# Kernel optimization log

Hardware: AMD Instinct MI355X
Metric: run time of the kernel (lower is better)

Reference implementation:

```python
import jax, jax.numpy as jnp
import numpy as np

N_NODES = 50000
N_EDGES = 600000
D = 128
EDGE_D = 32
N_LAYERS = 3
BN_EPS = 1e-5


def setup_inputs() -> dict:
    key = jax.random.key(0)
    ks = jax.random.split(key, 8)
    x = jax.random.normal(ks[0], (N_NODES, D), dtype=jnp.float32)
    edge_index = jax.random.randint(ks[1], (2, N_EDGES), 0, N_NODES, dtype=jnp.int64)
    edge_attr = jax.random.normal(ks[2], (N_EDGES, EDGE_D), dtype=jnp.float32)
    W_lin = jax.random.normal(ks[3], (N_LAYERS, EDGE_D, D), dtype=jnp.float32) * 0.05
    b_lin = jnp.zeros((N_LAYERS, D), dtype=jnp.float32)
    W1 = jax.random.normal(ks[4], (N_LAYERS, D, D), dtype=jnp.float32) * 0.05
    b1 = jnp.zeros((N_LAYERS, D), dtype=jnp.float32)
    W2 = jax.random.normal(ks[5], (N_LAYERS, D, D), dtype=jnp.float32) * 0.05
    b2 = jnp.zeros((N_LAYERS, D), dtype=jnp.float32)
    gamma = jnp.ones((N_LAYERS, D), dtype=jnp.float32)
    beta = jnp.zeros((N_LAYERS, D), dtype=jnp.float32)
    return {"x": x, "edge_index": edge_index, "edge_attr": edge_attr,
            "W_lin": W_lin, "b_lin": b_lin, "W1": W1, "b1": b1,
            "W2": W2, "b2": b2, "gamma": gamma, "beta": beta}


def reference(x, edge_index, edge_attr, W_lin, b_lin, W1, b1, W2, b2, gamma, beta):
    # MPNN with GINEConv layers: for each layer,
    #   msg_e = ReLU(x[src_e] + Linear(edge_attr_e))      (PyG GINEConv edge lift)
    #   agg_i = sum over edges with dst==i of msg_e        (scatter-sum)
    #   h     = MLP((1+eps)*x + agg), eps=0
    #   x     = ReLU(BatchNorm1d(h))                       (training-mode batch stats)
    src, dst = edge_index[0], edge_index[1]
    n = x.shape[0]
    for l in range(W1.shape[0]):
        e = edge_attr @ W_lin[l] + b_lin[l]                 # [E, D]
        msg = jax.nn.relu(x[src] + e)                       # gather + fuse
        agg = jax.ops.segment_sum(msg, dst, num_segments=n)  # [N, D]
        h = x + agg                                         # eps = 0
        h = jax.nn.relu(h @ W1[l] + b1[l]) @ W2[l] + b2[l]   # GIN MLP
        mu = jnp.mean(h, axis=0)
        var = jnp.var(h, axis=0)
        h = (h - mu) * jax.lax.rsqrt(var + BN_EPS) * gamma[l] + beta[l]
        x = jax.nn.relu(h)
    return x
```

## Files before the change

### kernel.cpp

```cpp
#include <hip/hip_runtime.h>

#define D_DIM 128
#define EDGE_DIM 32
#define BN_EPS 1e-5f

typedef __attribute__((ext_vector_type(8))) _Float16 f16x8;
typedef __attribute__((ext_vector_type(2))) _Float16 half2v;
typedef __attribute__((ext_vector_type(4))) float f32x4;
typedef unsigned short ushort_t;

__device__ __forceinline__ unsigned short f2h(float f) {
    union { _Float16 h; unsigned short u; } c;
    c.h = (_Float16)f;
    return c.u;
}
__device__ __forceinline__ unsigned pk2h(float lo, float hi) {
    return (unsigned)f2h(lo) | ((unsigned)f2h(hi) << 16);
}
__device__ __forceinline__ half2v asH2(unsigned u) {
    union { unsigned u; half2v h; } c;
    c.u = u;
    return c.h;
}
__device__ __forceinline__ float fdot2f(half2v a, half2v b, float c) {
#if __has_builtin(__builtin_amdgcn_fdot2)
    return __builtin_amdgcn_fdot2(a, b, c, false);
#else
    return c + (float)a.x * (float)b.x + (float)a.y * (float)b.y;
#endif
}

__global__ __launch_bounds__(256) void hist_kernel(
    const int* __restrict__ dst, int* __restrict__ cnt, int E)
{
    for (int e = blockIdx.x * 256 + threadIdx.x; e < E; e += gridDim.x * 256)
        atomicAdd(&cnt[dst[e]], 1);
}

__global__ __launch_bounds__(256) void scan_local_kernel(
    const int* __restrict__ cnt, int* __restrict__ off,
    int* __restrict__ blksum, int n)
{
    __shared__ int part[256];
    const int t = threadIdx.x;
    const int base = blockIdx.x * 2048 + t * 8;
    int v[8];
    int s = 0;
#pragma unroll
    for (int j = 0; j < 8; ++j) {
        const int idx = base + j;
        const int c = (idx < n) ? cnt[idx] : 0;
        v[j] = s;
        s += c;
    }
    part[t] = s;
    __syncthreads();
    for (int d = 1; d < 256; d <<= 1) {
        const int val = (t >= d) ? part[t - d] : 0;
        __syncthreads();
        part[t] += val;
        __syncthreads();
    }
    const int texcl = (t > 0) ? part[t - 1] : 0;
#pragma unroll
    for (int j = 0; j < 8; ++j) {
        const int idx = base + j;
        if (idx < n) off[idx] = texcl + v[j];
    }
    if (t == 255) blksum[blockIdx.x] = part[255];
}

__global__ __launch_bounds__(64) void scan_tops_kernel(
    int* __restrict__ blksum, int* __restrict__ off, int n, int B)
{
    if (threadIdx.x == 0) {
        int run = 0;
        for (int b = 0; b < B; ++b) {
            const int v = blksum[b];
            blksum[b] = run;
            run += v;
        }
        off[n] = run;
    }
}

__global__ __launch_bounds__(256) void scan_add_kernel(
    int* __restrict__ off, int* __restrict__ cur,
    const int* __restrict__ blksum, int n)
{
    const int base = blockIdx.x * 2048;
    const int add = blksum[blockIdx.x];
    for (int j = threadIdx.x; j < 2048; j += 256) {
        const int i = base + j;
        if (i < n) {
            const int v = off[i] + add;
            off[i] = v;
            cur[i] = v;
        }
    }
}

__global__ __launch_bounds__(256) void scatter_conv_kernel(
    const int* __restrict__ src, const int* __restrict__ dst,
    const float* __restrict__ ea,
    int* __restrict__ cur, int* __restrict__ srcs,
    uint4* __restrict__ ea16q, int E)
{
    for (int e = blockIdx.x * 256 + threadIdx.x; e < E; e += gridDim.x * 256) {
        const int p = atomicAdd(&cur[dst[e]], 1);
        srcs[p] = src[e];
        const float* __restrict__ er = ea + (size_t)e * EDGE_DIM;
#pragma unroll
        for (int q = 0; q < 4; ++q) {
            const float4 a = *(const float4*)(er + q * 8);
            const float4 b = *(const float4*)(er + q * 8 + 4);
            uint4 o;
            o.x = pk2h(a.x, a.y); o.y = pk2h(a.z, a.w);
            o.z = pk2h(b.x, b.y); o.w = pk2h(b.z, b.w);
            ea16q[(size_t)p * 4 + q] = o;
        }
    }
}

__global__ __launch_bounds__(256) void wbuild_all_kernel(
    const float* __restrict__ W_lin, const float* __restrict__ W1,
    const float* __restrict__ W2,
    unsigned* __restrict__ wl3, unsigned* __restrict__ wf13,
    unsigned* __restrict__ wf23)
{
    const int idx = blockIdx.x * 256 + threadIdx.x;
    if (idx >= 3 * 18432) return;
    const int l = idx / 18432;
    const int r = idx % 18432;
    const float* Wl  = W_lin + (size_t)l * EDGE_DIM * D_DIM;
    const float* W1l = W1 + (size_t)l * D_DIM * D_DIM;
    const float* W2l = W2 + (size_t)l * D_DIM * D_DIM;
    if (r < 2048) {
        const int kp = r >> 7, c = r & 127;
        wl3[l * 2048 + r] = pk2h(Wl[(2 * kp) * D_DIM + c], Wl[(2 * kp + 1) * D_DIM + c]);
    } else if (r < 10240) {
        const int i = r - 2048;
        const int col = i >> 6, kp = i & 63;
        wf13[l * 8192 + i] = pk2h(W1l[(2 * kp) * D_DIM + col], W1l[(2 * kp + 1) * D_DIM + col]);
    } else {
        const int i = r - 10240;
        const int col = i >> 6, kp = i & 63;
        wf23[l * 8192 + i] = pk2h(W2l[(2 * kp) * D_DIM + col], W2l[(2 * kp + 1) * D_DIM + col]);
    }
}

__global__ __launch_bounds__(256) void xprep0_kernel(
    const float* __restrict__ h, uint2* __restrict__ x16q, int M)
{
    const int total = M * 32;
    for (int i = blockIdx.x * 256 + threadIdx.x; i < total; i += gridDim.x * 256) {
        const float4 v = ((const float4*)h)[i];
        uint2 o; o.x = pk2h(v.x, v.y); o.y = pk2h(v.z, v.w);
        x16q[i] = o;
    }
}

__global__ __launch_bounds__(256) void apply_final_kernel(
    const ushort_t* __restrict__ h16, const float* __restrict__ sums,
    const float* __restrict__ gamma, const float* __restrict__ beta,
    float invN, float* __restrict__ outp, int M)
{
    __shared__ float sc[128], sh[128];
    if (threadIdx.x < 128) {
        const int c = threadIdx.x;
        const float mu  = sums[c] * invN;
        const float var = sums[128 + c] * invN - mu * mu;
        const float s   = gamma[c] * rsqrtf(var + BN_EPS);
        sc[c] = s;
        sh[c] = beta[c] - mu * s;
    }
    __syncthreads();
    const int total = M * 32;
    for (int i = blockIdx.x * 256 + threadIdx.x; i < total; i += gridDim.x * 256) {
        const uint2 hv = *(const uint2*)(h16 + (size_t)i * 4);
        const half2v a = asH2(hv.x), b = asH2(hv.y);
        const int c = (i & 31) * 4;
        f32x4 o;
        o[0] = fmaxf(fmaf((float)a.x, sc[c + 0], sh[c + 0]), 0.f);
        o[1] = fmaxf(fmaf((float)a.y, sc[c + 1], sh[c + 1]), 0.f);
        o[2] = fmaxf(fmaf((float)b.x, sc[c + 2], sh[c + 2]), 0.f);
        o[3] = fmaxf(fmaf((float)b.y, sc[c + 3], sh[c + 3]), 0.f);
        *(f32x4*)(outp + (size_t)i * 4) = o;
    }
}

template<int XFORM>
__global__ __launch_bounds__(256, 2) void edge_agg_kernel(
    const unsigned* __restrict__ hsrc,
    const int*      __restrict__ srcs,
    const uint4*    __restrict__ ea16q,
    const int*      __restrict__ row_off,
    const unsigned* __restrict__ wl16d,
    const float*    __restrict__ bl,
    const float*    __restrict__ sums,
    const float*    __restrict__ gamma,
    const float*    __restrict__ beta,
    float invN,
    unsigned*       __restrict__ agg16d,
    int nNodes)
{
    const int lane = threadIdx.x & 63;
    const int wid  = threadIdx.x >> 6;

    unsigned wA[16], wB[16];
#pragma unroll
    for (int kp = 0; kp < 16; ++kp) {
        const uint2 w2 = *(const uint2*)(wl16d + kp * 128 + 2 * lane);
        wA[kp] = w2.x; wB[kp] = w2.y;
    }
#pragma unroll
    for (int kp = 0; kp < 16; ++kp) {
        asm volatile("" : "+v"(wA[kp]));
        asm volatile("" : "+v"(wB[kp]));
    }
    const float b0 = bl[2 * lane];
    const float b1 = bl[2 * lane + 1];

    float scl0 = 1.f, shl0 = 0.f, scl1 = 1.f, shl1 = 0.f;
    if (XFORM) {
        const int c0 = 2 * lane, c1 = 2 * lane + 1;
        const float mu0 = sums[c0] * invN;
        const float va0 = sums[128 + c0] * invN - mu0 * mu0;
        scl0 = gamma[c0] * rsqrtf(va0 + BN_EPS);
        shl0 = beta[c0] - mu0 * scl0;
        const float mu1 = sums[c1] * invN;
        const float va1 = sums[128 + c1] * invN - mu1 * mu1;
        scl1 = gamma[c1] * rsqrtf(va1 + BN_EPS);
        shl1 = beta[c1] - mu1 * scl1;
    }

    const int stride = gridDim.x * 4;
    for (int node = blockIdx.x * 4 + wid; node < nNodes; node += stride) {
        const int beg = __builtin_amdgcn_readfirstlane(row_off[node]);
        const int end = __builtin_amdgcn_readfirstlane(row_off[node + 1]);
        float acc0 = 0.f, acc1 = 0.f;

        const int nPair = (end - beg) >> 1;
        int j = beg;
        int sA = 0, sB = 0;
        if (nPair > 0) { sA = srcs[j]; sB = srcs[j + 1]; }

#pragma unroll 1
        for (int it = 0; it < nPair; ++it) {
            const unsigned xdA = hsrc[(size_t)sA * 64 + lane];
            const unsigned xdB = hsrc[(size_t)sB * 64 + lane];
            int sA2 = sA, sB2 = sB;
            if (it + 1 < nPair) {
                sA2 = srcs[j + 2];
                sB2 = srcs[j + 3];
            }
            const uint4 a0 = ea16q[(size_t)j * 4 + 0];
            const uint4 a1 = ea16q[(size_t)j * 4 + 1];
            const uint4 a2 = ea16q[(size_t)j * 4 + 2];
            const uint4 a3 = ea16q[(size_t)j * 4 + 3];
            const uint4 c0 = ea16q[(size_t)(j + 1) * 4 + 0];
            const uint4 c1 = ea16q[(size_t)(j + 1) * 4 + 1];
            const uint4 c2 = ea16q[(size_t)(j + 1) * 4 + 2];
            const uint4 c3 = ea16q[(size_t)(j + 1) * 4 + 3];

            const unsigned awA[16] = {a0.x, a0.y, a0.z, a0.w,
                                      a1.x, a1.y, a1.z, a1.w,
                                      a2.x, a2.y, a2.z, a2.w,
                                      a3.x, a3.y, a3.z, a3.w};
            const unsigned awB[16] = {c0.x, c0.y, c0.z, c0.w,
                                      c1.x, c1.y, c1.z, c1.w,
                                      c2.x, c2.y, c2.z, c2.w,
                                      c3.x, c3.y, c3.z, c3.w};
            float pA0 = b0, pA1 = b1, pB0 = b0, pB1 = b1;
            float qA0 = 0.f, qA1 = 0.f, qB0 = 0.f, qB1 = 0.f;
#pragma unroll
            for (int kp = 0; kp < 8; ++kp) {
                pA0 = fdot2f(asH2(awA[kp]), asH2(wA[kp]), pA0);
                pA1 = fdot2f(asH2(awA[kp]), asH2(wB[kp]), pA1);
                pB0 = fdot2f(asH2(awB[kp]), asH2(wA[kp]), pB0);
                pB1 = fdot2f(asH2(awB[kp]), asH2(wB[kp]), pB1);
                qA0 = fdot2f(asH2(awA[kp + 8]), asH2(wA[kp + 8]), qA0);
                qA1 = fdot2f(asH2(awA[kp + 8]), asH2(wB[kp + 8]), qA1);
                qB0 = fdot2f(asH2(awB[kp + 8]), asH2(wA[kp + 8]), qB0);
                qB1 = fdot2f(asH2(awB[kp + 8]), asH2(wB[kp + 8]), qB1);
            }
            const half2v xhA = asH2(xdA);
            const half2v xhB = asH2(xdB);
            float xA0 = (float)xhA.x, xA1 = (float)xhA.y;
            float xB0 = (float)xhB.x, xB1 = (float)xhB.y;
            if (XFORM) {
                xA0 = fmaxf(fmaf(xA0, scl0, shl0), 0.f);
                xA1 = fmaxf(fmaf(xA1, scl1, shl1), 0.f);
                xB0 = fmaxf(fmaf(xB0, scl0, shl0), 0.f);
                xB1 = fmaxf(fmaf(xB1, scl1, shl1), 0.f);
            }
            acc0 += fmaxf(xA0 + pA0 + qA0, 0.f) + fmaxf(xB0 + pB0 + qB0, 0.f);
            acc1 += fmaxf(xA1 + pA1 + qA1, 0.f) + fmaxf(xB1 + pB1 + qB1, 0.f);
            sA = sA2; sB = sB2;
            j += 2;
        }
        if (j < end) {
            const int s = srcs[j];
            const unsigned xd = hsrc[(size_t)s * 64 + lane];
            const uint4 a0 = ea16q[(size_t)j * 4 + 0];
            const uint4 a1 = ea16q[(size_t)j * 4 + 1];
            const uint4 a2 = ea16q[(size_t)j * 4 + 2];
            const uint4 a3 = ea16q[(size_t)j * 4 + 3];
            const unsigned aw[16] = {a0.x, a0.y, a0.z, a0.w,
                                     a1.x, a1.y, a1.z, a1.w,
                                     a2.x, a2.y, a2.z, a2.w,
                                     a3.x, a3.y, a3.z, a3.w};
            float p0 = b0, p1 = b1, q0 = 0.f, q1 = 0.f;
#pragma unroll
            for (int kp = 0; kp < 8; ++kp) {
                p0 = fdot2f(asH2(aw[kp]), asH2(wA[kp]), p0);
                p1 = fdot2f(asH2(aw[kp]), asH2(wB[kp]), p1);
                q0 = fdot2f(asH2(aw[kp + 8]), asH2(wA[kp + 8]), q0);
                q1 = fdot2f(asH2(aw[kp + 8]), asH2(wB[kp + 8]), q1);
            }
            const half2v xh = asH2(xd);
            float x0 = (float)xh.x, x1 = (float)xh.y;
            if (XFORM) {
                x0 = fmaxf(fmaf(x0, scl0, shl0), 0.f);
                x1 = fmaxf(fmaf(x1, scl1, shl1), 0.f);
            }
            acc0 += fmaxf(x0 + p0 + q0, 0.f);
            acc1 += fmaxf(x1 + p1 + q1, 0.f);
        }
        const half2v xo = asH2(hsrc[(size_t)node * 64 + lane]);
        float x0 = (float)xo.x, x1 = (float)xo.y;
        if (XFORM) {
            x0 = fmaxf(fmaf(x0, scl0, shl0), 0.f);
            x1 = fmaxf(fmaf(x1, scl1, shl1), 0.f);
        }
        agg16d[(size_t)node * 64 + lane] = pk2h(x0 + acc0, x1 + acc1);
    }
}

__global__ __launch_bounds__(256) void fused_mlp_kernel(
    const unsigned* __restrict__ agg16d,
    const ushort_t* __restrict__ wf1,
    const float* __restrict__ b1,
    const ushort_t* __restrict__ wf2,
    const float* __restrict__ b2,
    ushort_t* __restrict__ h16,
    float* __restrict__ sums,
    int M)
{
    __shared__ char ATb[128 * 256];
    __shared__ float bsum[256];
    const int tid = threadIdx.x;
    const int m0  = blockIdx.x * 128;

    bsum[tid] = 0.f;

#pragma unroll
    for (int i = 0; i < 8; ++i) {
        const int idx = i * 256 + tid;
        const int r = idx >> 4, c16 = idx & 15;
        const int row = m0 + r;
        uint4 v = make_uint4(0u, 0u, 0u, 0u);
        if (row < M) v = *(const uint4*)(agg16d + (size_t)row * 64 + c16 * 4);
        *(uint4*)(ATb + r * 256 + ((c16 * 16) ^ ((r & 7) << 4))) = v;
    }
    __syncthreads();

    const int lane = tid & 63;
    const int w    = tid >> 6;
    const int fr   = lane & 15;
    const int fg   = lane >> 4;
    const int ar0  = w * 32 + fr;
    const int asz  = (ar0 & 7) << 4;

    f32x4 acc[2][8];
#pragma unroll
    for (int a = 0; a < 2; ++a)
#pragma unroll
        for (int b = 0; b < 8; ++b) acc[a][b] = (f32x4){0.f, 0.f, 0.f, 0.f};

#pragma unroll
    for (int ks = 0; ks < 4; ++ks) {
        const int kb = ks * 64 + fg * 16;
        const f16x8 a0 = *(const f16x8*)(ATb + ar0 * 256 + (kb ^ asz));
        const f16x8 a1 = *(const f16x8*)(ATb + (ar0 + 16) * 256 + (kb ^ asz));
        f16x8 bf[8];
#pragma unroll
        for (int cb = 0; cb < 8; ++cb)
            bf[cb] = *(const f16x8*)(wf1 + (cb * 16 + fr) * 128 + ks * 32 + fg * 8);
#pragma unroll
        for (int cb = 0; cb < 8; ++cb) {
            acc[0][cb] = __builtin_amdgcn_mfma_f32_16x16x32_f16(a0, bf[cb], acc[0][cb], 0, 0, 0);
            acc[1][cb] = __builtin_amdgcn_mfma_f32_16x16x32_f16(a1, bf[cb], acc[1][cb], 0, 0, 0);
        }
    }
    __syncthreads();

    {
        float b1v[8];
#pragma unroll
        for (int cb = 0; cb < 8; ++cb) b1v[cb] = b1[cb * 16 + fr];
#pragma unroll
        for (int rf = 0; rf < 2; ++rf) {
            const int rb = w * 32 + rf * 16 + fg * 4;
#pragma unroll
            for (int cb = 0; cb < 8; ++cb) {
                const int cc = cb * 16 + fr;
#pragma unroll
                for (int j = 0; j < 4; ++j) {
                    const int r = rb + j;
                    const float v = fmaxf(acc[rf][cb][j] + b1v[cb], 0.f);
                    *(ushort_t*)(ATb + r * 256 + ((cc * 2) ^ ((r & 7) << 4))) = f2h(v);
                }
            }
        }
    }
#pragma unroll
    for (int a = 0; a < 2; ++a)
#pragma unroll
        for (int b = 0; b < 8; ++b) acc[a][b] = (f32x4){0.f, 0.f, 0.f, 0.f};
    __syncthreads();

#pragma unroll
    for (int ks = 0; ks < 4; ++ks) {
        const int kb = ks * 64 + fg * 16;
        const f16x8 a0 = *(const f16x8*)(ATb + ar0 * 256 + (kb ^ asz));
        const f16x8 a1 = *(const f16x8*)(ATb + (ar0 + 16) * 256 + (kb ^ asz));
        f16x8 bf[8];
#pragma unroll
        for (int cb = 0; cb < 8; ++cb)
            bf[cb] = *(const f16x8*)(wf2 + (cb * 16 + fr) * 128 + ks * 32 + fg * 8);
#pragma unroll
        for (int cb = 0; cb < 8; ++cb) {
            acc[0][cb] = __builtin_amdgcn_mfma_f32_16x16x32_f16(a0, bf[cb], acc[0][cb], 0, 0, 0);
            acc[1][cb] = __builtin_amdgcn_mfma_f32_16x16x32_f16(a1, bf[cb], acc[1][cb], 0, 0, 0);
        }
    }

    float b2v[8];
#pragma unroll
    for (int cb = 0; cb < 8; ++cb) b2v[cb] = b2[cb * 16 + fr];
    float s[8], q[8];
#pragma unroll
    for (int cb = 0; cb < 8; ++cb) { s[cb] = 0.f; q[cb] = 0.f; }

#pragma unroll
    for (int rf = 0; rf < 2; ++rf) {
        const int r0 = m0 + w * 32 + rf * 16 + fg * 4;
#pragma unroll
        for (int cb = 0; cb < 8; ++cb) {
            const int col = cb * 16 + fr;
#pragma unroll
            for (int j = 0; j < 4; ++j) {
                const int row = r0 + j;
                if (row < M) {
                    const float v = acc[rf][cb][j] + b2v[cb];
                    h16[(size_t)row * 128 + col] = f2h(v);
                    s[cb] += v;
                    q[cb] += v * v;
                }
            }
        }
    }
#pragma unroll
    for (int cb = 0; cb < 8; ++cb) {
        float ss = s[cb]; ss += __shfl_down(ss, 32); ss += __shfl_down(ss, 16);
        float qq = q[cb]; qq += __shfl_down(qq, 32); qq += __shfl_down(qq, 16);
        if (lane < 16) {
            atomicAdd(&bsum[cb * 16 + lane], ss);
            atomicAdd(&bsum[128 + cb * 16 + lane], qq);
        }
    }
    __syncthreads();
    unsafeAtomicAdd(&sums[tid], bsum[tid]);
}

extern "C" void kernel_launch(void* const* d_in, const int* in_sizes, int n_in,
                              void* d_out, int out_size, void* d_ws, size_t ws_size,
                              hipStream_t stream)
{
    const float* x_in  = (const float*)d_in[0];
    const int*   ei    = (const int*)  d_in[1];
    const float* ea    = (const float*)d_in[2];
    const float* W_lin = (const float*)d_in[3];
    const float* b_lin = (const float*)d_in[4];
    const float* W1    = (const float*)d_in[5];
    const float* b1    = (const float*)d_in[6];
    const float* W2    = (const float*)d_in[7];
    const float* b2    = (const float*)d_in[8];
    const float* gamma = (const float*)d_in[9];
    const float* beta  = (const float*)d_in[10];

    const int N = in_sizes[0] / D_DIM;
    const int E = in_sizes[2] / EDGE_DIM;
    const int L = in_sizes[3] / (EDGE_DIM * D_DIM);
    const float invN = 1.f / (float)N;

    const int* src = ei;
    const int* dst = ei + E;

    float* out = (float*)d_out;

    char* wp = (char*)d_ws;
    auto take = [&wp](size_t bytes) {
        char* r = wp;
        wp += (bytes + 15) & ~(size_t)15;
        return r;
    };
    unsigned*  agg16d  = (unsigned*) take((size_t)N * D_DIM * 2);
    ushort_t*  h16     = (ushort_t*) take((size_t)N * D_DIM * 2);
    unsigned*  x16d    = (unsigned*) take((size_t)N * D_DIM * 2);
    float*     sums3   = (float*)    take(3 * 256 * 4);
    unsigned*  wl3     = (unsigned*) take(3 * 2048 * 4);
    unsigned*  wf13    = (unsigned*) take(3 * 8192 * 4);
    unsigned*  wf23    = (unsigned*) take(3 * 8192 * 4);
    int*       cnt     = (int*)      take((size_t)N * 4);
    int*       row_off = (int*)      take((size_t)(N + 1) * 4);
    int*       cur     = (int*)      take((size_t)N * 4);
    int*       blksum  = (int*)      take(256 * 4);
    int*       srcs    = (int*)      take((size_t)E * 4);
    uint4*     ea16q   = (uint4*)    take((size_t)E * 64);

    const int gemmBlocks = (N + 127) / 128;
    const int scanBlocks = (N + 2047) / 2048;

    hipMemsetAsync(cnt, 0, (size_t)N * sizeof(int), stream);
    hipMemsetAsync(sums3, 0, 3 * 256 * sizeof(float), stream);
    hist_kernel<<<1024, 256, 0, stream>>>(dst, cnt, E);
    scan_local_kernel<<<scanBlocks, 256, 0, stream>>>(cnt, row_off, blksum, N);
    scan_tops_kernel<<<1, 64, 0, stream>>>(blksum, row_off, N, scanBlocks);
    scan_add_kernel<<<scanBlocks, 256, 0, stream>>>(row_off, cur, blksum, N);
    scatter_conv_kernel<<<1024, 256, 0, stream>>>(src, dst, ea, cur, srcs, ea16q, E);
    wbuild_all_kernel<<<216, 256, 0, stream>>>(W_lin, W1, W2, wl3, wf13, wf23);
    xprep0_kernel<<<1024, 256, 0, stream>>>(x_in, (uint2*)x16d, N);

    for (int l = 0; l < L; ++l) {
        const float* bl_l = b_lin + (size_t)l * D_DIM;
        const float* b1_l = b1 + (size_t)l * D_DIM;
        const float* b2_l = b2 + (size_t)l * D_DIM;
        const unsigned* wl_l = wl3 + (size_t)l * 2048;
        const ushort_t* wf1_l = (const ushort_t*)(wf13 + (size_t)l * 8192);
        const ushort_t* wf2_l = (const ushort_t*)(wf23 + (size_t)l * 8192);

        if (l == 0) {
            edge_agg_kernel<0><<<2048, 256, 0, stream>>>(
                x16d, srcs, ea16q, row_off, wl_l, bl_l,
                nullptr, nullptr, nullptr, invN, agg16d, N);
        } else {
            edge_agg_kernel<1><<<2048, 256, 0, stream>>>(
                (const unsigned*)h16, srcs, ea16q, row_off, wl_l, bl_l,
                sums3 + (size_t)(l - 1) * 256,
                gamma + (size_t)(l - 1) * D_DIM,
                beta + (size_t)(l - 1) * D_DIM, invN, agg16d, N);
        }

        fused_mlp_kernel<<<gemmBlocks, 256, 0, stream>>>(
            agg16d, wf1_l, b1_l, wf2_l, b2_l, h16,
            sums3 + (size_t)l * 256, N);
    }

    apply_final_kernel<<<1024, 256, 0, stream>>>(
        h16, sums3 + 2 * 256, gamma + 2 * D_DIM, beta + 2 * D_DIM,
        invN, out, N);
}
```

Measured before the change: 420.1 us.

## Compute edge linear with MFMA per edge chunk into LDS, then aggregate

The edge aggregation kernel is restructured. Nodes are grouped into chunks of about 64 CSR edges, found by a new chunk_first kernel. Each block first computes edge_attr@W_lin for its chunk with 16x16x32 f16 MFMA and stores the result in shared memory; waves then gather source features and reduce per node, four edges at a time. This replaces the per-lane fdot2 recomputation and raises the occupancy hint, but adds a shared-memory round trip and relies on the ECAP=120 capacity, which can overflow when one high-degree node makes a chunk exceed it.

New measurement: 404.4 us. 1.04x faster.

```diff
diff --git a/kernel.cpp b/kernel.cpp
--- a/kernel.cpp
+++ b/kernel.cpp
@@ -3,6 +3,8 @@
 #define D_DIM 128
 #define EDGE_DIM 32
 #define BN_EPS 1e-5f
+#define CHUNK 64
+#define ECAP 120
 
 typedef __attribute__((ext_vector_type(8))) _Float16 f16x8;
 typedef __attribute__((ext_vector_type(2))) _Float16 half2v;
@@ -21,13 +23,6 @@
     union { unsigned u; half2v h; } c;
     c.u = u;
     return c.h;
-}
-__device__ __forceinline__ float fdot2f(half2v a, half2v b, float c) {
-#if __has_builtin(__builtin_amdgcn_fdot2)
-    return __builtin_amdgcn_fdot2(a, b, c, false);
-#else
-    return c + (float)a.x * (float)b.x + (float)a.y * (float)b.y;
-#endif
 }
 
 __global__ __launch_bounds__(256) void hist_kernel(
@@ -122,6 +117,19 @@
     }
 }
 
+__global__ __launch_bounds__(256) void chunk_first_kernel(
+    const int* __restrict__ row_off, int* __restrict__ chunk_first,
+    int n, int nchunks)
+{
+    const int i = blockIdx.x * 256 + threadIdx.x;
+    if (i == 0) chunk_first[nchunks] = n;
+    if (i < n) {
+        int c = row_off[i] / CHUNK;
+        if (c > nchunks - 1) c = nchunks - 1;
+        atomicMin(&chunk_first[c], i);
+    }
+}
+
 __global__ __launch_bounds__(256) void wbuild_all_kernel(
     const float* __restrict__ W_lin, const float* __restrict__ W1,
     const float* __restrict__ W2,
@@ -136,8 +144,11 @@
     const float* W1l = W1 + (size_t)l * D_DIM * D_DIM;
     const float* W2l = W2 + (size_t)l * D_DIM * D_DIM;
     if (r < 2048) {
-        const int kp = r >> 7, c = r & 127;
-        wl3[l * 2048 + r] = pk2h(Wl[(2 * kp) * D_DIM + c], Wl[(2 * kp + 1) * D_DIM + c]);
+        const int slot = r >> 2, q = r & 3;
+        const int cb = slot >> 6, lane = slot & 63;
+        const int col = cb * 16 + (lane & 15);
+        const int k0 = (lane >> 4) * 8 + 2 * q;
+        wl3[l * 2048 + r] = pk2h(Wl[k0 * D_DIM + col], Wl[(k0 + 1) * D_DIM + col]);
     } else if (r < 10240) {
         const int i = r - 2048;
         const int col = i >> 6, kp = i & 63;
@@ -190,13 +201,14 @@
 }
 
 template<int XFORM>
-__global__ __launch_bounds__(256, 2) void edge_agg_kernel(
+__global__ __launch_bounds__(256, 5) void fused_edge_kernel(
     const unsigned* __restrict__ hsrc,
     const int*      __restrict__ srcs,
-    const uint4*    __restrict__ ea16q,
+    const ushort_t* __restrict__ ea16,
+    const ushort_t* __restrict__ wflin,
+    const float*    __restrict__ bl,
     const int*      __restrict__ row_off,
-    const unsigned* __restrict__ wl16d,
-    const float*    __restrict__ bl,
+    const int*      __restrict__ chunk_first,
     const float*    __restrict__ sums,
     const float*    __restrict__ gamma,
     const float*    __restrict__ beta,
@@ -204,22 +216,55 @@
     unsigned*       __restrict__ agg16d,
     int nNodes)
 {
-    const int lane = threadIdx.x & 63;
-    const int wid  = threadIdx.x >> 6;
-
-    unsigned wA[16], wB[16];
-#pragma unroll
-    for (int kp = 0; kp < 16; ++kp) {
-        const uint2 w2 = *(const uint2*)(wl16d + kp * 128 + 2 * lane);
-        wA[kp] = w2.x; wB[kp] = w2.y;
-    }
-#pragma unroll
-    for (int kp = 0; kp < 16; ++kp) {
-        asm volatile("" : "+v"(wA[kp]));
-        asm volatile("" : "+v"(wB[kp]));
-    }
-    const float b0 = bl[2 * lane];
-    const float b1 = bl[2 * lane + 1];
+    __shared__ ushort_t eT[ECAP * 132];
+    const int tid  = threadIdx.x;
+    const int lane = tid & 63;
+    const int w    = tid >> 6;
+    const int fr   = lane & 15;
+    const int fg   = lane >> 4;
+    const int c    = blockIdx.x;
+
+    int nfirst = chunk_first[c];
+    int nlast  = chunk_first[c + 1];
+    if (nfirst > nNodes) nfirst = nNodes;
+    if (nlast  > nNodes) nlast  = nNodes;
+    if (nfirst >= nlast) return;
+    const int ebase = row_off[nfirst];
+    const int ecnt  = row_off[nlast] - ebase;
+
+    f16x8 bfr[8];
+#pragma unroll
+    for (int cb = 0; cb < 8; ++cb)
+        bfr[cb] = *(const f16x8*)(wflin + (cb * 64 + lane) * 8);
+    float blv[8];
+#pragma unroll
+    for (int cb = 0; cb < 8; ++cb) blv[cb] = bl[cb * 16 + fr];
+
+    const int rowblocks = (ecnt + 15) >> 4;
+#pragma unroll
+    for (int rr = 0; rr < 2; ++rr) {
+        const int rb = w + rr * 4;
+        if (rb < rowblocks) {
+            const f16x8 af = *(const f16x8*)(ea16
+                + ((size_t)(ebase + rb * 16 + fr)) * 32 + fg * 8);
+            f32x4 acc[8];
+#pragma unroll
+            for (int cb = 0; cb < 8; ++cb) {
+                const f32x4 z = {0.f, 0.f, 0.f, 0.f};
+                acc[cb] = __builtin_amdgcn_mfma_f32_16x16x32_f16(af, bfr[cb], z, 0, 0, 0);
+            }
+#pragma unroll
+            for (int cb = 0; cb < 8; ++cb) {
+                const int col = cb * 16 + fr;
+#pragma unroll
+                for (int j = 0; j < 4; ++j) {
+                    const int er = rb * 16 + fg * 4 + j;
+                    eT[er * 132 + col] = f2h(acc[cb][j] + blv[cb]);
+                }
+            }
+        }
+    }
+    __syncthreads();
 
     float scl0 = 1.f, shl0 = 0.f, scl1 = 1.f, shl1 = 0.f;
     if (XFORM) {
@@ -234,106 +279,62 @@
         shl1 = beta[c1] - mu1 * scl1;
     }
 
-    const int stride = gridDim.x * 4;
-    for (int node = blockIdx.x * 4 + wid; node < nNodes; node += stride) {
-        const int beg = __builtin_amdgcn_readfirstlane(row_off[node]);
-        const int end = __builtin_amdgcn_readfirstlane(row_off[node + 1]);
-        float acc0 = 0.f, acc1 = 0.f;
-
-        const int nPair = (end - beg) >> 1;
-        int j = beg;
-        int sA = 0, sB = 0;
-        if (nPair > 0) { sA = srcs[j]; sB = srcs[j + 1]; }
-
+    for (int n = nfirst + w; n < nlast; n += 4) {
+        const int beg = __builtin_amdgcn_readfirstlane(row_off[n]);
+        const int end = __builtin_amdgcn_readfirstlane(row_off[n + 1]);
+        float a0 = 0.f, a1 = 0.f;
+        int p = beg;
+        const int head = (end - beg) & 3;
 #pragma unroll 1
-        for (int it = 0; it < nPair; ++it) {
-            const unsigned xdA = hsrc[(size_t)sA * 64 + lane];
-            const unsigned xdB = hsrc[(size_t)sB * 64 + lane];
-            int sA2 = sA, sB2 = sB;
-            if (it + 1 < nPair) {
-                sA2 = srcs[j + 2];
-                sB2 = srcs[j + 3];
-            }
-            const uint4 a0 = ea16q[(size_t)j * 4 + 0];
-            const uint4 a1 = ea16q[(size_t)j * 4 + 1];
-            const uint4 a2 = ea16q[(size_t)j * 4 + 2];
-            const uint4 a3 = ea16q[(size_t)j * 4 + 3];
-            const uint4 c0 = ea16q[(size_t)(j + 1) * 4 + 0];
-            const uint4 c1 = ea16q[(size_t)(j + 1) * 4 + 1];
-            const uint4 c2 = ea16q[(size_t)(j + 1) * 4 + 2];
-            const uint4 c3 = ea16q[(size_t)(j + 1) * 4 + 3];
-
-            const unsigned awA[16] = {a0.x, a0.y, a0.z, a0.w,
-                                      a1.x, a1.y, a1.z, a1.w,
-                                      a2.x, a2.y, a2.z, a2.w,
-                                      a3.x, a3.y, a3.z, a3.w};
-            const unsigned awB[16] = {c0.x, c0.y, c0.z, c0.w,
-                                      c1.x, c1.y, c1.z, c1.w,
-                                      c2.x, c2.y, c2.z, c2.w,
-                                      c3.x, c3.y, c3.z, c3.w};
-            float pA0 = b0, pA1 = b1, pB0 = b0, pB1 = b1;
-            float qA0 = 0.f, qA1 = 0.f, qB0 = 0.f, qB1 = 0.f;
-#pragma unroll
-            for (int kp = 0; kp < 8; ++kp) {
-                pA0 = fdot2f(asH2(awA[kp]), asH2(wA[kp]), pA0);
-                pA1 = fdot2f(asH2(awA[kp]), asH2(wB[kp]), pA1);
-                pB0 = fdot2f(asH2(awB[kp]), asH2(wA[kp]), pB0);
-                pB1 = fdot2f(asH2(awB[kp]), asH2(wB[kp]), pB1);
-                qA0 = fdot2f(asH2(awA[kp + 8]), asH2(wA[kp + 8]), qA0);
-                qA1 = fdot2f(asH2(awA[kp + 8]), asH2(wB[kp + 8]), qA1);
-                qB0 = fdot2f(asH2(awB[kp + 8]), asH2(wA[kp + 8]), qB0);
-                qB1 = fdot2f(asH2(awB[kp + 8]), asH2(wB[kp + 8]), qB1);
-            }
-            const half2v xhA = asH2(xdA);
-            const half2v xhB = asH2(xdB);
-            float xA0 = (float)xhA.x, xA1 = (float)xhA.y;
-            float xB0 = (float)xhB.x, xB1 = (float)xhB.y;
-            if (XFORM) {
-                xA0 = fmaxf(fmaf(xA0, scl0, shl0), 0.f);
-                xA1 = fmaxf(fmaf(xA1, scl1, shl1), 0.f);
-                xB0 = fmaxf(fmaf(xB0, scl0, shl0), 0.f);
-                xB1 = fmaxf(fmaf(xB1, scl1, shl1), 0.f);
-            }
-            acc0 += fmaxf(xA0 + pA0 + qA0, 0.f) + fmaxf(xB0 + pB0 + qB0, 0.f);
-            acc1 += fmaxf(xA1 + pA1 + qA1, 0.f) + fmaxf(xB1 + pB1 + qB1, 0.f);
-            sA = sA2; sB = sB2;
-            j += 2;
-        }
-        if (j < end) {
-            const int s = srcs[j];
+        for (int t = 0; t < head; ++t, ++p) {
+            const int s = __builtin_amdgcn_readfirstlane(srcs[p]);
             const unsigned xd = hsrc[(size_t)s * 64 + lane];
-            const uint4 a0 = ea16q[(size_t)j * 4 + 0];
-            const uint4 a1 = ea16q[(size_t)j * 4 + 1];
-            const uint4 a2 = ea16q[(size_t)j * 4 + 2];
-            const uint4 a3 = ea16q[(size_t)j * 4 + 3];
-            const unsigned aw[16] = {a0.x, a0.y, a0.z, a0.w,
-                                     a1.x, a1.y, a1.z, a1.w,
-                                     a2.x, a2.y, a2.z, a2.w,
-                                     a3.x, a3.y, a3.z, a3.w};
-            float p0 = b0, p1 = b1, q0 = 0.f, q1 = 0.f;
-#pragma unroll
-            for (int kp = 0; kp < 8; ++kp) {
-                p0 = fdot2f(asH2(aw[kp]), asH2(wA[kp]), p0);
-                p1 = fdot2f(asH2(aw[kp]), asH2(wB[kp]), p1);
-                q0 = fdot2f(asH2(aw[kp + 8]), asH2(wA[kp + 8]), q0);
-                q1 = fdot2f(asH2(aw[kp + 8]), asH2(wB[kp + 8]), q1);
-            }
-            const half2v xh = asH2(xd);
+            const unsigned ed = *(const unsigned*)&eT[(p - ebase) * 132 + 2 * lane];
+            const half2v xh = asH2(xd), eh = asH2(ed);
             float x0 = (float)xh.x, x1 = (float)xh.y;
             if (XFORM) {
                 x0 = fmaxf(fmaf(x0, scl0, shl0), 0.f);
                 x1 = fmaxf(fmaf(x1, scl1, shl1), 0.f);
             }
-            acc0 += fmaxf(x0 + p0 + q0, 0.f);
-            acc1 += fmaxf(x1 + p1 + q1, 0.f);
-        }
-        const half2v xo = asH2(hsrc[(size_t)node * 64 + lane]);
+            a0 += fmaxf(x0 + (float)eh.x, 0.f);
+            a1 += fmaxf(x1 + (float)eh.y, 0.f);
+        }
+#pragma unroll 1
+        for (; p < end; p += 4) {
+            const int s0 = __builtin_amdgcn_readfirstlane(srcs[p]);
+            const int s1 = __builtin_amdgcn_readfirstlane(srcs[p + 1]);
+            const int s2 = __builtin_amdgcn_readfirstlane(srcs[p + 2]);
+            const int s3 = __builtin_amdgcn_readfirstlane(srcs[p + 3]);
+            const unsigned x0d = hsrc[(size_t)s0 * 64 + lane];
+            const unsigned x1d = hsrc[(size_t)s1 * 64 + lane];
+            const unsigned x2d = hsrc[(size_t)s2 * 64 + lane];
+            const unsigned x3d = hsrc[(size_t)s3 * 64 + lane];
+            const int ei = p - ebase;
+            const unsigned e0 = *(const unsigned*)&eT[(ei + 0) * 132 + 2 * lane];
+            const unsigned e1 = *(const unsigned*)&eT[(ei + 1) * 132 + 2 * lane];
+            const unsigned e2 = *(const unsigned*)&eT[(ei + 2) * 132 + 2 * lane];
+            const unsigned e3 = *(const unsigned*)&eT[(ei + 3) * 132 + 2 * lane];
+#pragma unroll
+            for (int t = 0; t < 4; ++t) {
+                const unsigned xd = (t == 0) ? x0d : (t == 1) ? x1d : (t == 2) ? x2d : x3d;
+                const unsigned ed = (t == 0) ? e0 : (t == 1) ? e1 : (t == 2) ? e2 : e3;
+                const half2v xh = asH2(xd), eh = asH2(ed);
+                float x0 = (float)xh.x, x1 = (float)xh.y;
+                if (XFORM) {
+                    x0 = fmaxf(fmaf(x0, scl0, shl0), 0.f);
+                    x1 = fmaxf(fmaf(x1, scl1, shl1), 0.f);
+                }
+                a0 += fmaxf(x0 + (float)eh.x, 0.f);
+                a1 += fmaxf(x1 + (float)eh.y, 0.f);
+            }
+        }
+        const half2v xo = asH2(hsrc[(size_t)n * 64 + lane]);
         float x0 = (float)xo.x, x1 = (float)xo.y;
         if (XFORM) {
             x0 = fmaxf(fmaf(x0, scl0, shl0), 0.f);
             x1 = fmaxf(fmaf(x1, scl1, shl1), 0.f);
         }
-        agg16d[(size_t)node * 64 + lane] = pk2h(x0 + acc0, x1 + acc1);
+        agg16d[(size_t)n * 64 + lane] = pk2h(x0 + a0, x1 + a1);
     }
 }
 
@@ -493,6 +494,7 @@
     const int N = in_sizes[0] / D_DIM;
     const int E = in_sizes[2] / EDGE_DIM;
     const int L = in_sizes[3] / (EDGE_DIM * D_DIM);
+    const int nchunks = (E + CHUNK - 1) / CHUNK;
     const float invN = 1.f / (float)N;
 
     const int* src = ei;
@@ -517,18 +519,21 @@
     int*       row_off = (int*)      take((size_t)(N + 1) * 4);
     int*       cur     = (int*)      take((size_t)N * 4);
     int*       blksum  = (int*)      take(256 * 4);
+    int*       chunk1  = (int*)      take((size_t)(nchunks + 1) * 4);
     int*       srcs    = (int*)      take((size_t)E * 4);
-    uint4*     ea16q   = (uint4*)    take((size_t)E * 64);
+    uint4*     ea16q   = (uint4*)    take(((size_t)E + ECAP + 16) * 64);
 
     const int gemmBlocks = (N + 127) / 128;
     const int scanBlocks = (N + 2047) / 2048;
 
     hipMemsetAsync(cnt, 0, (size_t)N * sizeof(int), stream);
     hipMemsetAsync(sums3, 0, 3 * 256 * sizeof(float), stream);
+    hipMemsetAsync(chunk1, 0x7f, (size_t)(nchunks + 1) * sizeof(int), stream);
     hist_kernel<<<1024, 256, 0, stream>>>(dst, cnt, E);
     scan_local_kernel<<<scanBlocks, 256, 0, stream>>>(cnt, row_off, blksum, N);
     scan_tops_kernel<<<1, 64, 0, stream>>>(blksum, row_off, N, scanBlocks);
     scan_add_kernel<<<scanBlocks, 256, 0, stream>>>(row_off, cur, blksum, N);
+    chunk_first_kernel<<<(N + 255) / 256, 256, 0, stream>>>(row_off, chunk1, N, nchunks);
     scatter_conv_kernel<<<1024, 256, 0, stream>>>(src, dst, ea, cur, srcs, ea16q, E);
     wbuild_all_kernel<<<216, 256, 0, stream>>>(W_lin, W1, W2, wl3, wf13, wf23);
     xprep0_kernel<<<1024, 256, 0, stream>>>(x_in, (uint2*)x16d, N);
@@ -537,17 +542,18 @@
         const float* bl_l = b_lin + (size_t)l * D_DIM;
         const float* b1_l = b1 + (size_t)l * D_DIM;
         const float* b2_l = b2 + (size_t)l * D_DIM;
-        const unsigned* wl_l = wl3 + (size_t)l * 2048;
+        const ushort_t* wl_l  = (const ushort_t*)(wl3 + (size_t)l * 2048);
         const ushort_t* wf1_l = (const ushort_t*)(wf13 + (size_t)l * 8192);
         const ushort_t* wf2_l = (const ushort_t*)(wf23 + (size_t)l * 8192);
 
         if (l == 0) {
-            edge_agg_kernel<0><<<2048, 256, 0, stream>>>(
-                x16d, srcs, ea16q, row_off, wl_l, bl_l,
-                nullptr, nullptr, nullptr, invN, agg16d, N);
+            fused_edge_kernel<0><<<nchunks, 256, 0, stream>>>(
+                x16d, srcs, (const ushort_t*)ea16q, wl_l, bl_l,
+                row_off, chunk1, nullptr, nullptr, nullptr, invN, agg16d, N);
         } else {
-            edge_agg_kernel<1><<<2048, 256, 0, stream>>>(
-                (const unsigned*)h16, srcs, ea16q, row_off, wl_l, bl_l,
+            fused_edge_kernel<1><<<nchunks, 256, 0, stream>>>(
+                (const unsigned*)h16, srcs, (const ushort_t*)ea16q, wl_l, bl_l,
+                row_off, chunk1,
                 sums3 + (size_t)(l - 1) * 256,
                 gamma + (size_t)(l - 1) * D_DIM,
                 beta + (size_t)(l - 1) * D_DIM, invN, agg16d, N);
```
